# Kernel optimization log

Hardware: AMD Instinct MI355X
Metric: run time of the kernel (lower is better)

The kernel has to match this reference:

```python
import jax, jax.numpy as jnp
import numpy as np

SIGMA = 1.0
E_THETA = 0.1
E_ALPHA = 1.0
T = 750   # hardcoded by the original loop `for i in range(750)`
W = 11    # window width, loop `for j in range(11)`


def _pad(a):
    # Replicates the torch padding: [first*6, a, last*5] -> length T+11.
    # (The torch code writes last-6 slots then overwrites index T+5 with the
    #  middle slice; net effect is 6 copies of first, 5 copies of last.)
    return jnp.concatenate(
        [jnp.repeat(a[:, :1], 6, axis=1), a, jnp.repeat(a[:, -1:], 5, axis=1)],
        axis=1,
    )


def setup_inputs() -> dict:
    key = jax.random.key(0)
    k1, k2 = jax.random.split(key)
    B = 4096
    return {
        "actioness": jax.random.uniform(k1, (B, T), dtype=jnp.float32),
        "actioness_2": jax.random.uniform(k2, (B, T), dtype=jnp.float32),
    }


def reference(actioness, actioness_2):
    a0, a2 = actioness, actioness_2      # [B, T]
    p0, p2 = _pad(a0), _pad(a2)          # [B, T+11]
    win0 = jnp.stack([p0[:, j:j + T] for j in range(W)], axis=-1)  # [B, T, 11]
    win2 = jnp.stack([p2[:, j:j + T] for j in range(W)], axis=-1)  # [B, T, 11]
    # Gaussian-style weight from actioness similarity
    w = jnp.exp(-jnp.abs(a0[:, :, None] - win0) / (2.0 * SIGMA * SIGMA))
    loss = jnp.sum(w * jnp.abs(a2[:, :, None] - win2))
    # L2 regularizer: per-row L2 norm of the difference, summed over batch
    loss = loss + E_THETA * jnp.sum(jnp.linalg.norm(a0 - a2, axis=1))
    return loss * E_ALPHA
```

## Files before the change

### kernel.cpp

```cpp
#include <hip/hip_runtime.h>
#include <math.h>


#define T_LEN 750
#define W_LEN 11
#define PAD_T 761
#define BLK 256
#define CPT 3
#define WIN (CPT + 10)

__global__ __launch_bounds__(BLK) void actloss_partial(
    const float* __restrict__ a0, const float* __restrict__ a2,
    float* __restrict__ partials)
{
    __shared__ float s0[PAD_T];
    __shared__ float s2[PAD_T];

    const int b   = blockIdx.x;
    const int tid = threadIdx.x;
    const float* __restrict__ g0 = a0 + (size_t)b * T_LEN;
    const float* __restrict__ g2 = a2 + (size_t)b * T_LEN;

    for (int k = tid; k < PAD_T; k += BLK) {
        int src = k - 6;
        src = src < 0 ? 0 : (src > T_LEN - 1 ? T_LEN - 1 : src);
        s0[k] = g0[src];
        s2[k] = g2[src];
    }
    __syncthreads();

    float loss = 0.0f;
    float sq   = 0.0f;

    if (tid < T_LEN / CPT) {
        const int i0 = tid * CPT;
        float r0[WIN], r2[WIN];
#pragma unroll
        for (int k = 0; k < WIN; ++k) {
            r0[k] = s0[i0 + k];
            r2[k] = s2[i0 + k];
        }
#pragma unroll
        for (int ci = 0; ci < CPT; ++ci) {
            const float c0 = r0[ci + 6];
            const float c2 = r2[ci + 6];
#pragma unroll
            for (int j = 0; j < W_LEN; ++j) {
                const float wv = __expf(-0.5f * fabsf(c0 - r0[ci + j]));
                loss = fmaf(wv, fabsf(c2 - r2[ci + j]), loss);
            }
            const float d = c0 - c2;
            sq = fmaf(d, d, sq);
        }
    }

#pragma unroll
    for (int off = 32; off > 0; off >>= 1) {
        loss += __shfl_down(loss, off, 64);
        sq   += __shfl_down(sq,   off, 64);
    }
    __shared__ float rl[BLK / 64], rs[BLK / 64];
    const int wid  = tid >> 6;
    const int lane = tid & 63;
    if (lane == 0) { rl[wid] = loss; rs[wid] = sq; }
    __syncthreads();
    if (tid == 0) {
        float L = 0.0f, S = 0.0f;
#pragma unroll
        for (int w = 0; w < BLK / 64; ++w) { L += rl[w]; S += rs[w]; }
        partials[b] = L + 0.1f * sqrtf(S);
    }
}

__global__ __launch_bounds__(BLK) void actloss_final(
    const float* __restrict__ partials, int n, float* __restrict__ out)
{
    float v = 0.0f;
    for (int k = threadIdx.x; k < n; k += BLK) v += partials[k];
#pragma unroll
    for (int off = 32; off > 0; off >>= 1) v += __shfl_down(v, off, 64);
    __shared__ float r[BLK / 64];
    const int wid  = threadIdx.x >> 6;
    const int lane = threadIdx.x & 63;
    if (lane == 0) r[wid] = v;
    __syncthreads();
    if (threadIdx.x == 0) {
        float s = 0.0f;
#pragma unroll
        for (int w = 0; w < BLK / 64; ++w) s += r[w];
        out[0] = s;
    }
}

extern "C" void kernel_launch(void* const* d_in, const int* in_sizes, int n_in,
                              void* d_out, int out_size, void* d_ws, size_t ws_size,
                              hipStream_t stream)
{
    const float* a0 = (const float*)d_in[0];
    const float* a2 = (const float*)d_in[1];
    float* out      = (float*)d_out;
    float* partials = (float*)d_ws;
    const int B = in_sizes[0] / T_LEN;

    actloss_partial<<<B, BLK, 0, stream>>>(a0, a2, partials);
    actloss_final<<<1, BLK, 0, stream>>>(partials, B, out);
}
```

Measured before the change: 79.40 us.

## Exploit window symmetry to halve exp evaluations and handle padding analytically

The weight and the absolute difference are both symmetric in the pair, so the kernel now visits each unordered pair at forward offsets 1..6 only. Offsets 1..4 are weighted twice and offsets 5..6 once, which cuts the exp and abs work per element roughly in half. The replicated-edge padding contributions are recovered in closed form by one extra thread using multiplicity factors. It also switches to the raw exp2 builtin with a prescaled log2e constant. This adds fragile boundary bookkeeping and changes the floating-point summation order.

```diff
diff --git a/kernel.cpp b/kernel.cpp
--- a/kernel.cpp
+++ b/kernel.cpp
@@ -3,56 +3,73 @@
 
 
 #define T_LEN 750
-#define W_LEN 11
-#define PAD_T 761
-#define BLK 256
-#define CPT 3
-#define WIN (CPT + 10)
+#define BLK   256
+#define CPT   3
+#define NACT  (T_LEN / CPT)
+#define SPAD  756
+#define L2E_HALF 0.72134752044f
 
 __global__ __launch_bounds__(BLK) void actloss_partial(
     const float* __restrict__ a0, const float* __restrict__ a2,
     float* __restrict__ partials)
 {
-    __shared__ float s0[PAD_T];
-    __shared__ float s2[PAD_T];
+    __shared__ float s0[SPAD];
+    __shared__ float s2[SPAD];
 
     const int b   = blockIdx.x;
     const int tid = threadIdx.x;
     const float* __restrict__ g0 = a0 + (size_t)b * T_LEN;
     const float* __restrict__ g2 = a2 + (size_t)b * T_LEN;
 
-    for (int k = tid; k < PAD_T; k += BLK) {
-        int src = k - 6;
-        src = src < 0 ? 0 : (src > T_LEN - 1 ? T_LEN - 1 : src);
+    for (int k = tid; k < SPAD; k += BLK) {
+        const int src = k < T_LEN ? k : T_LEN - 1;
         s0[k] = g0[src];
         s2[k] = g2[src];
     }
     __syncthreads();
 
-    float loss = 0.0f;
-    float sq   = 0.0f;
+    float loss1 = 0.0f;
+    float loss2 = 0.0f;
+    float sq    = 0.0f;
 
-    if (tid < T_LEN / CPT) {
+    if (tid < NACT) {
         const int i0 = tid * CPT;
-        float r0[WIN], r2[WIN];
+        float r0[CPT + 6], r2[CPT + 6];
 #pragma unroll
-        for (int k = 0; k < WIN; ++k) {
+        for (int k = 0; k < CPT + 6; ++k) {
             r0[k] = s0[i0 + k];
             r2[k] = s2[i0 + k];
         }
 #pragma unroll
         for (int ci = 0; ci < CPT; ++ci) {
-            const float c0 = r0[ci + 6];
-            const float c2 = r2[ci + 6];
+            const float c0 = r0[ci];
+            const float c2 = r2[ci];
 #pragma unroll
-            for (int j = 0; j < W_LEN; ++j) {
-                const float wv = __expf(-0.5f * fabsf(c0 - r0[ci + j]));
-                loss = fmaf(wv, fabsf(c2 - r2[ci + j]), loss);
+            for (int k = 1; k <= 6; ++k) {
+                const float wv  = __builtin_amdgcn_exp2f(
+                                      -L2E_HALF * fabsf(c0 - r0[ci + k]));
+                float ad2 = fabsf(c2 - r2[ci + k]);
+                ad2 = (i0 + ci + k < T_LEN) ? ad2 : 0.0f;
+                if (k <= 4) loss2 = fmaf(wv, ad2, loss2);
+                else        loss1 = fmaf(wv, ad2, loss1);
             }
             const float d = c0 - c2;
             sq = fmaf(d, d, sq);
         }
+    } else if (tid == NACT) {
+#pragma unroll
+        for (int i = 1; i <= 5; ++i) {
+            const float wv = __builtin_amdgcn_exp2f(-L2E_HALF * fabsf(s0[i] - s0[0]));
+            loss1 = fmaf(wv * (float)(6 - i), fabsf(s2[i] - s2[0]), loss1);
+        }
+#pragma unroll
+        for (int i = 746; i <= 748; ++i) {
+            const float wv = __builtin_amdgcn_exp2f(-L2E_HALF * fabsf(s0[i] - s0[T_LEN - 1]));
+            loss1 = fmaf(wv * (float)(i - 745), fabsf(s2[i] - s2[T_LEN - 1]), loss1);
+        }
     }
+
+    float loss = fmaf(2.0f, loss2, loss1);
 
 #pragma unroll
     for (int off = 32; off > 0; off >>= 1) {
@@ -80,9 +97,7 @@
 #pragma unroll
     for (int off = 32; off > 0; off >>= 1) v += __shfl_down(v, off, 64);
     __shared__ float r[BLK / 64];
-    const int wid  = threadIdx.x >> 6;
-    const int lane = threadIdx.x & 63;
-    if (lane == 0) r[wid] = v;
+    if ((threadIdx.x & 63) == 0) r[threadIdx.x >> 6] = v;
     __syncthreads();
     if (threadIdx.x == 0) {
         float s = 0.0f;
```

After: 77.43 us. 2.5% less time.
